# Kernel tuning notes

Measured on AMD Instinct MI355X. Metric: run time of the kernel, lower is better.

## Reference

```python
import jax, jax.numpy as jnp
import numpy as np

B, F, R, P, C = 2048, 64, 32, 16, 128  # batch, nfeature(dsym), nrole, npattern, dcontext
TAU = 2.0  # posn_attender sharpness


def setup_inputs() -> dict:
    key = jax.random.key(0)
    ks = jax.random.split(key, 16)
    w = lambda k, shape, s=0.05: jax.random.normal(k, shape, jnp.float32) * s
    z = lambda shape: jnp.zeros(shape, jnp.float32)
    return {
        "form": jax.random.normal(ks[0], (B, F, R), jnp.float32),
        "context": jax.random.normal(ks[1], (B, C), jnp.float32),
        "mod_W": w(ks[2], (C, P * 6)), "mod_b": z((P * 6,)),
        "wch_W": w(ks[3], (C, P * F)), "wch_b": z((P * F,)),
        "wdl_W": w(ks[4], (C, P)), "wdl_b": z((P,)),
        "wep_W": w(ks[5], (C, P * 4)), "wep_b": z((P * 4,)),
        "vch_W": w(ks[6], (C, P * F)), "vch_b": z((P * F,)),
        "vep_W": w(ks[7], (C, P * F * 4)), "vep_b": z((P * F * 4,)),
        "wnc_W": w(ks[8], (C, F)), "wnc_b": z((F,)),
        "wnd_W": w(ks[9], (C, 1)), "wnd_b": z((1,)),
        "wne_W": w(ks[10], (C, 1)), "wne_b": z((1,)),
        "m_W": w(ks[11], (3, C, P * F)), "m_Wb": z((3, P * F)),
        "mb_W": w(ks[12], (3, C, P)), "mb_b": z((3, P)),
    }


def _forward(form, context, mod_W, mod_b, wch_W, wch_b, wdl_W, wdl_b,
             wep_W, wep_b, vch_W, vch_b, vep_W, vep_b,
             wnc_W, wnc_b, wnd_W, wnd_b, wne_W, wne_b,
             m_W, m_Wb, mb_W, mb_b):
    nb = form.shape[0]
    lin = lambda W, b: context @ W + b

    # context-conditioned rule weights
    mod = jax.nn.softmax(lin(mod_W, mod_b).reshape(nb, P, 6), axis=-1)
    w_chng = mod[..., 0:1] * lin(wch_W, wch_b).reshape(nb, P, F)
    w_deln = mod[..., 1:2] * lin(wdl_W, wdl_b).reshape(nb, P, 1)
    w_epen = mod[..., 2:] * lin(wep_W, wep_b).reshape(nb, P, 4)
    v_chng = lin(vch_W, vch_b).reshape(nb, P, F)
    v_epen = lin(vep_W, vep_b).reshape(nb, P, F, 4)
    w_nochng = jnp.exp(lin(wnc_W, wnc_b))   # (B, F)
    w_nodeln = jnp.exp(lin(wnd_W, wnd_b))   # (B, 1)
    w_noepen = jnp.exp(lin(wne_W, wne_b))   # (B, 1)

    # Matcher3: trigram (prev, cur, next) feature matching; log-prob summed then exp'd
    prev = jnp.pad(form[:, :, :-1], ((0, 0), (0, 0), (1, 0)))
    nxt = jnp.pad(form[:, :, 1:], ((0, 0), (0, 0), (0, 1)))
    forms3 = jnp.stack([prev, form, nxt], 0)                                   # (3,B,F,R)
    Wk = (jnp.einsum('bc,kcn->kbn', context, m_W) + m_Wb[:, None, :]).reshape(3, nb, P, F)
    bk = jnp.einsum('bc,kcp->kbp', context, mb_W) + mb_b[:, None, :]
    score = jnp.einsum('kbpf,kbfr->kbpr', Wk, forms3) + bk[..., None]
    match = jnp.exp(jnp.sum(jax.nn.log_sigmoid(score), axis=0))                # (B,P,R)

    positions = jnp.arange(R, dtype=form.dtype)

    def posn_attn(posn):  # (B,1) soft position -> (B,R) radial-basis attention
        return jax.nn.softmax(-TAU * (posn - positions[None, :]) ** 2, axis=-1)

    def bind(out, x, attn):  # soft write symbol x at attended role
        a = attn[:, None, :]
        return out * (1.0 - a) + x[:, :, None] * a

    def epen(out, posn, match_i, we_p, ve_p):
        we = match_i * we_p                                                    # (B,P)
        p = jax.nn.sigmoid(jnp.sum(we, 1, keepdims=True) - w_noepen)           # (B,1)
        v = jnp.sum(jax.nn.relu(we)[..., None] * ve_p, 1)                      # (B,F)
        out_ = bind(out, v, posn_attn(posn))
        out = p[..., None] * out_ + (1.0 - p[..., None]) * out
        return out, posn + p

    def step(carry, x):
        out, posn = carry
        sym_i, match_i = x  # (B,F), (B,P)
        # epenthesis before
        out, posn = epen(out, posn, match_i, w_epen[..., 0], v_epen[..., 0])
        # feature change + deletion
        wc = match_i[..., None] * w_chng                                       # (B,P,F)
        p_chng = jax.nn.sigmoid(jnp.sum(wc, 1) - w_nochng)                     # (B,F)
        vc = jnp.sum(jax.nn.relu(wc) * v_chng, 1)                              # (B,F)
        sym = sym_i + p_chng * (vc - sym_i)
        out_ = bind(out, sym, posn_attn(posn))
        wd = match_i[..., None] * w_deln                                       # (B,P,1)
        p_deln = jax.nn.sigmoid(jnp.sum(wd, 1) - w_nodeln)                     # (B,1)
        out = (1.0 - p_deln[..., None]) * out_ + p_deln[..., None] * out
        posn = posn + (1.0 - p_deln)
        # epenthesis after
        out, posn = epen(out, posn, match_i, w_epen[..., 2], v_epen[..., 2])
        return (out, posn), None

    carry0 = (jnp.zeros((nb, F, R), form.dtype), jnp.zeros((nb, 1), form.dtype))
    xs = (jnp.moveaxis(form, 2, 0), jnp.moveaxis(match, 2, 0))
    (out, _), _ = jax.lax.scan(step, carry0, xs)
    return out


def reference(form, context, mod_W, mod_b, wch_W, wch_b, wdl_W, wdl_b,
              wep_W, wep_b, vch_W, vch_b, vep_W, vep_b,
              wnc_W, wnc_b, wnd_W, wnd_b, wne_W, wne_b,
              m_W, m_Wb, mb_W, mb_b):
    return _forward(form, context, mod_W, mod_b, wch_W, wch_b, wdl_W, wdl_b,
                    wep_W, wep_b, vch_W, vch_b, vep_W, vep_b,
                    wnc_W, wnc_b, wnd_W, wnd_b, wne_W, wne_b,
                    m_W, m_Wb, mb_W, mb_b)
```

## Files before the change

kernel.cpp:

```cpp
#include <hip/hip_runtime.h>

#define B_ 2048
#define NTOT 7426
#define YSTRIDE 7432
#define WSTRIDE 8192

typedef unsigned short u16;
typedef unsigned int   u32;
typedef __attribute__((ext_vector_type(2))) float v2f;

__device__ __forceinline__ float bfu(u16 u) {
    u32 i = ((u32)u) << 16; float f; __builtin_memcpy(&f, &i, 4); return f;
}
__device__ __forceinline__ float bflo(u32 w) {
    u32 i = w << 16; float f; __builtin_memcpy(&f, &i, 4); return f;
}
__device__ __forceinline__ float bfhi(u32 w) {
    u32 i = w & 0xffff0000u; float f; __builtin_memcpy(&f, &i, 4); return f;
}
__device__ __forceinline__ u16 f2bf(float v) {
    u32 iv; __builtin_memcpy(&iv, &v, 4);
    u32 r = (iv + 0x7fffu + ((iv >> 16) & 1u)) >> 16;
    return (u16)r;
}
__device__ __forceinline__ float sigm(float x) { return 1.f / (1.f + __expf(-x)); }
__device__ __forceinline__ float lsg(float x) {
    return fminf(x, 0.f) - log1pf(__expf(-fabsf(x)));
}

template<bool F32> __device__ __forceinline__ float LD(const void* p, int e) {
    if (F32) return ((const float*)p)[e];
    return bfu(((const u16*)p)[e]);
}
template<bool F32> __device__ __forceinline__ float2 LD2(const void* p, int e) {
    if (F32) { const float* q = (const float*)p; return make_float2(q[e], q[e + 1]); }
    u32 w = ((const u32*)p)[e >> 1];
    return make_float2(bflo(w), bfhi(w));
}
template<bool F32> __device__ __forceinline__ float4 LD4(const void* p, int e) {
    if (F32) return ((const float4*)p)[e >> 2];
    uint2 w = ((const uint2*)p)[e >> 2];
    return make_float4(bflo(w.x), bfhi(w.x), bflo(w.y), bfhi(w.y));
}
template<bool F32> __device__ __forceinline__ void ST(void* p, int e, float v) {
    if (F32) ((float*)p)[e] = v; else ((u16*)p)[e] = f2bf(v);
}

struct Args {
    const void *form, *ctx;
    const void *mod_W, *mod_b, *wch_W, *wch_b, *wdl_W, *wdl_b, *wep_W, *wep_b;
    const void *vch_W, *vch_b, *vep_W, *vep_b;
    const void *wnc_W, *wnc_b, *wnd_W, *wnd_b, *wne_W, *wne_b;
    const void *m_W, *m_Wb, *mb_W, *mb_b;
    void* outp;
};

__device__ __forceinline__ int probe_is_f32(const void* ctx, int t, int* flag_s) {
    if (t == 0) {
        int sane = 0;
        const u16* q = (const u16*)ctx;
        for (int i = 0; i < 64; ++i) {
            u16 u = q[2 * i];
            int ex = (u >> 7) & 0xFF;
            sane += (u == 0 || (ex >= 112 && ex <= 143)) ? 1 : 0;
        }
        *flag_s = (sane < 32) ? 1 : 0;
    }
    __syncthreads();
    return *flag_s;
}

struct PD { const void* p0; int off; int st; int mode; float b0, b1; };

template<bool F32>
__device__ __forceinline__ void resolve(const Args& A, int n0, PD& d) {
    if (n0 < 96) {
        d.mode = 0; d.p0 = A.mod_W; d.off = n0; d.st = 96;
        float2 b = LD2<F32>(A.mod_b, n0); d.b0 = b.x; d.b1 = b.y;
    } else if (n0 < 1120) {
        int j = n0 - 96;
        d.mode = 0; d.p0 = A.wch_W; d.off = j; d.st = 1024;
        float2 b = LD2<F32>(A.wch_b, j); d.b0 = b.x; d.b1 = b.y;
    } else if (n0 < 2144) {
        int j = n0 - 1120;
        d.mode = 0; d.p0 = A.vch_W; d.off = j; d.st = 1024;
        float2 b = LD2<F32>(A.vch_b, j); d.b0 = b.x; d.b1 = b.y;
    } else if (n0 < 4192) {
        int u = (n0 - 2144) >> 1;
        d.mode = 1; d.p0 = A.vep_W; d.off = 4 * u; d.st = 4096;
        float4 b = LD4<F32>(A.vep_b, 4 * u); d.b0 = b.x; d.b1 = b.z;
    } else if (n0 < 7264) {
        int i = n0 - 4192; int k = i >> 10, j = i & 1023;
        d.mode = 0; d.p0 = A.m_W; d.off = k * 131072 + j; d.st = 1024;
        float2 b = LD2<F32>(A.m_Wb, k * 1024 + j); d.b0 = b.x; d.b1 = b.y;
    } else if (n0 < 7312) {
        int i = n0 - 7264; int k = i >> 4, p = i & 15;
        d.mode = 0; d.p0 = A.mb_W; d.off = k * 2048 + p; d.st = 16;
        float2 b = LD2<F32>(A.mb_b, k * 16 + p); d.b0 = b.x; d.b1 = b.y;
    } else if (n0 < 7344) {
        int u = (n0 - 7312) >> 1;
        d.mode = 1; d.p0 = A.wep_W; d.off = 4 * u; d.st = 64;
        float4 b = LD4<F32>(A.wep_b, 4 * u); d.b0 = b.x; d.b1 = b.z;
    } else if (n0 < 7360) {
        int j = n0 - 7344;
        d.mode = 0; d.p0 = A.wdl_W; d.off = j; d.st = 16;
        float2 b = LD2<F32>(A.wdl_b, j); d.b0 = b.x; d.b1 = b.y;
    } else if (n0 < 7424) {
        int j = n0 - 7360;
        d.mode = 0; d.p0 = A.wnc_W; d.off = j; d.st = 64;
        float2 b = LD2<F32>(A.wnc_b, j); d.b0 = b.x; d.b1 = b.y;
    } else if (n0 == 7424) {
        d.mode = 2; d.p0 = A.wnd_W; d.off = 0; d.st = 1;
        d.b0 = LD<F32>(A.wnd_b, 0); d.b1 = LD<F32>(A.wne_b, 0);
    } else {
        d.mode = 3; d.p0 = A.mod_W; d.off = 0; d.st = 0; d.b0 = 0.f; d.b1 = 0.f;
    }
}

template<bool F32>
__device__ __forceinline__ v2f fetchw(const PD& d, const Args& A, int c) {
    if (d.mode == 0) {
        float2 w = LD2<F32>(d.p0, d.off + c * d.st);
        v2f r; r.x = w.x; r.y = w.y; return r;
    } else if (d.mode == 1) {
        float4 q = LD4<F32>(d.p0, d.off + c * d.st);
        v2f r; r.x = q.x; r.y = q.z; return r;
    } else if (d.mode == 2) {
        v2f r; r.x = LD<F32>(A.wnd_W, c); r.y = LD<F32>(A.wne_W, c); return r;
    }
    v2f r; r.x = 0.f; r.y = 0.f; return r;
}

template<bool F32>
__device__ void repack_body(int pid, const Args& A, float* Wcat, float* bcat) {
    int n0 = 2 * (pid & 4095);
    int c  = pid >> 12;
    PD d;
    resolve<F32>(A, n0, d);
    v2f w = fetchw<F32>(d, A, c);
    float2 s; s.x = w.x; s.y = w.y;
    *(float2*)(Wcat + (size_t)c * WSTRIDE + n0) = s;
    if (c == 0) { bcat[n0] = d.b0; bcat[n0 + 1] = d.b1; }
}

__global__ __launch_bounds__(256) void repack_kernel(Args A, float* Wcat, float* bcat) {
    __shared__ int dt_s;
    const int t = threadIdx.x;
    int isf32 = probe_is_f32(A.ctx, t, &dt_s);
    int pid = blockIdx.x * 256 + t;
    if (isf32) repack_body<true>(pid, A, Wcat, bcat);
    else       repack_body<false>(pid, A, Wcat, bcat);
}

template<bool F32>
__device__ void gemm4_body(float* ctx_s, int t, int blk, const void* __restrict__ ctx,
                           const float* __restrict__ Wcat, const float* __restrict__ bcat,
                           float* __restrict__ Y) {
    const int cb = blk & 7;
    const int mb = (blk >> 3) * 8;

    {
        int m = t >> 5, c0 = (t & 31) * 4;
        float4 v = LD4<F32>(ctx, (mb + m) * 128 + c0);
        *(float4*)&ctx_s[m * 128 + c0] = v;
    }
    __syncthreads();

    const int n0 = cb * 1024 + 4 * t;
    const float4* W4 = (const float4*)Wcat;
    const int wcol = n0 >> 2;

    float4 bv = *(const float4*)(bcat + n0);
    v2f acc[8][2];
    #pragma unroll
    for (int m = 0; m < 8; ++m) {
        acc[m][0].x = bv.x; acc[m][0].y = bv.y;
        acc[m][1].x = bv.z; acc[m][1].y = bv.w;
    }

    float4 w[4];
    #pragma unroll
    for (int j = 0; j < 4; ++j) w[j] = W4[(size_t)j * 2048 + wcol];

    #pragma unroll 1
    for (int c4 = 0; c4 < 128; c4 += 4) {
        float4 wn[4];
        if (c4 + 4 < 128) {
            #pragma unroll
            for (int j = 0; j < 4; ++j) wn[j] = W4[(size_t)(c4 + 4 + j) * 2048 + wcol];
        }
        #pragma unroll
        for (int m = 0; m < 8; ++m) {
            float4 cv = *(const float4*)&ctx_s[m * 128 + c4];
            float cs[4] = {cv.x, cv.y, cv.z, cv.w};
            #pragma unroll
            for (int j = 0; j < 4; ++j) {
                v2f cc; cc.x = cs[j]; cc.y = cs[j];
                v2f w01; w01.x = w[j].x; w01.y = w[j].y;
                v2f w23; w23.x = w[j].z; w23.y = w[j].w;
                acc[m][0] += cc * w01;
                acc[m][1] += cc * w23;
            }
        }
        #pragma unroll
        for (int j = 0; j < 4; ++j) w[j] = wn[j];
    }

    if (n0 < YSTRIDE) {
        #pragma unroll
        for (int m = 0; m < 8; ++m) {
            float4 s;
            s.x = acc[m][0].x; s.y = acc[m][0].y; s.z = acc[m][1].x; s.w = acc[m][1].y;
            *(float4*)(Y + (size_t)(mb + m) * YSTRIDE + n0) = s;
        }
    }
}

__global__ __launch_bounds__(256) void gemm4_kernel(Args A, const float* Wcat,
                                                    const float* bcat, float* Y) {
    __shared__ float ctx_s[8 * 128];
    __shared__ int dt_s;
    const int t = threadIdx.x, blk = blockIdx.x;
    int isf32 = probe_is_f32(A.ctx, t, &dt_s);
    if (isf32) gemm4_body<true>(ctx_s, t, blk, A.ctx, Wcat, bcat, Y);
    else       gemm4_body<false>(ctx_s, t, blk, A.ctx, Wcat, bcat, Y);
}

template<bool F32>
__device__ void gemm_body(float (*ctx_s)[128], int t, int blk, const Args& A, float* Y) {
    const int cb = blk & 3;
    const int mb = (blk >> 2) * 8;
    {
        int m = t >> 5, c0 = (t & 31) * 4;
        float4 v = LD4<F32>(A.ctx, (mb + m) * 128 + c0);
        ctx_s[m][c0] = v.x; ctx_s[m][c0 + 1] = v.y; ctx_s[m][c0 + 2] = v.z; ctx_s[m][c0 + 3] = v.w;
    }
    __syncthreads();
    PD d[4]; int n0[4];
    #pragma unroll
    for (int i = 0; i < 4; ++i) { n0[i] = cb * 2048 + i * 512 + 2 * t; resolve<F32>(A, n0[i], d[i]); }
    v2f acc[4][8];
    #pragma unroll
    for (int i = 0; i < 4; ++i)
        #pragma unroll
        for (int m = 0; m < 8; ++m) { acc[i][m].x = d[i].b0; acc[i][m].y = d[i].b1; }
    for (int c4 = 0; c4 < 32; ++c4) {
        float cv[8][4];
        #pragma unroll
        for (int m = 0; m < 8; ++m) *(float4*)cv[m] = *(const float4*)&ctx_s[m][c4 * 4];
        #pragma unroll
        for (int j = 0; j < 4; ++j) {
            int c = c4 * 4 + j;
            v2f w[4];
            #pragma unroll
            for (int i = 0; i < 4; ++i) w[i] = fetchw<F32>(d[i], A, c);
            #pragma unroll
            for (int m = 0; m < 8; ++m) {
                v2f cvv; cvv.x = cv[m][j]; cvv.y = cv[m][j];
                #pragma unroll
                for (int i = 0; i < 4; ++i) acc[i][m] += cvv * w[i];
            }
        }
    }
    #pragma unroll
    for (int i = 0; i < 4; ++i) {
        if (d[i].mode < 3) {
            #pragma unroll
            for (int m = 0; m < 8; ++m) {
                float2 s; s.x = acc[i][m].x; s.y = acc[i][m].y;
                *(float2*)(Y + (size_t)(mb + m) * YSTRIDE + n0[i]) = s;
            }
        }
    }
}

__global__ __launch_bounds__(256) void gemm_kernel(Args A, float* Y) {
    __shared__ float ctx_s[8][128];
    __shared__ int dt_s;
    const int t = threadIdx.x, blk = blockIdx.x;
    int isf32 = probe_is_f32(A.ctx, t, &dt_s);
    if (isf32) gemm_body<true>(ctx_s, t, blk, A, Y);
    else       gemm_body<false>(ctx_s, t, blk, A, Y);
}

struct __align__(16) ScanSmem {
    float U[6144];
    float V[3072];
    float match_s[512];
    float wnc_s[64];
    float wep0_s[16], wep2_s[16], wdl_s[16];
    float coef_s[96];
    float sc_s[2];
};

template<bool F32>
__device__ void scan_body(ScanSmem& S, int t, int b, const Args& A, const float* __restrict__ Y) {
    float* Wk_s   = S.U;
    float* bk_s   = S.U + 3072;
    float* modl   = S.U + 3120;
    float* form_s = S.U + 3312;
    float* xtab   = S.U;
    float* wch_s  = S.V;
    float* vch_s  = S.V + 1024;
    float* rlI    = S.V + 2048;
    float* gtab   = S.V;

    const float* Yr = Y + (size_t)b * YSTRIDE;
    const float4* Y4 = (const float4*)Yr;

    const int f_own = t & 63;
    const int fq    = t >> 6;

    const float2* vep2p = (const float2*)(Yr + 2144);
    v2f vepf[16];
    #pragma unroll
    for (int p = 0; p < 16; ++p) {
        float2 v = vep2p[p * 64 + f_own];
        vepf[p].x = v.x; vepf[p].y = v.y;
    }

    {
        int e0 = b * 2048 + t * 8;
        float4 x = LD4<F32>(A.form, e0);
        float4 y = LD4<F32>(A.form, e0 + 4);
        int f = t >> 2, r0 = (t & 3) * 8;
        float* dst = form_s + f * 33 + r0;
        dst[0] = x.x; dst[1] = x.y; dst[2] = x.z; dst[3] = x.w;
        dst[4] = y.x; dst[5] = y.y; dst[6] = y.z; dst[7] = y.w;
    }
    for (int i = t; i < 768; i += 256) ((float4*)Wk_s)[i] = Y4[1048 + i];
    if (t < 12) ((float4*)bk_s)[t] = Y4[1816 + t];
    if (t < 24) ((float4*)modl)[t] = Y4[t];
    ((float4*)wch_s)[t] = Y4[24 + t];
    ((float4*)vch_s)[t] = Y4[280 + t];
    if (t < 16) {
        S.wep0_s[t] = Yr[7312 + 2 * t];
        S.wep2_s[t] = Yr[7312 + 2 * t + 1];
        S.wdl_s[t]  = Yr[7344 + t];
    } else if (t >= 32 && t < 96) {
        S.wnc_s[t - 32] = __expf(Yr[7360 + (t - 32)]);
    } else if (t >= 96 && t < 98) {
        S.sc_s[t - 96] = __expf(Yr[7424 + (t - 96)]);
    }
    __syncthreads();

    if (t < 16) {
        float v[6]; float mx = -1e30f;
        #pragma unroll
        for (int j = 0; j < 6; ++j) { v[j] = modl[t * 6 + j]; mx = fmaxf(mx, v[j]); }
        float s = 0.f;
        #pragma unroll
        for (int j = 0; j < 6; ++j) { v[j] = __expf(v[j] - mx); s += v[j]; }
        float inv = 1.f / s;
        #pragma unroll
        for (int j = 0; j < 6; ++j) modl[t * 6 + j] = v[j] * inv;
    }
    __syncthreads();

    if (t < 16) {
        S.wep0_s[t] *= modl[t * 6 + 2];
        S.wep2_s[t] *= modl[t * 6 + 4];
        S.wdl_s[t]  *= modl[t * 6 + 1];
    }
    for (int i = t; i < 1024; i += 256) wch_s[i] *= modl[(i >> 6) * 6];

    const int my_r = t & 31;
    #pragma unroll 1
    for (int it = 0; it < 2; ++it) {
        int idx = t + 256 * it;
        int p = idx >> 5, r = idx & 31;
        float s0 = bk_s[p], s1 = bk_s[16 + p], s2 = bk_s[32 + p];
        const float4* w0 = (const float4*)(Wk_s + p * 64);
        const float4* w1 = (const float4*)(Wk_s + (16 + p) * 64);
        const float4* w2 = (const float4*)(Wk_s + (32 + p) * 64);
        for (int f4 = 0; f4 < 16; ++f4) {
            float a0[4], a1[4], a2[4];
            *(float4*)a0 = w0[f4]; *(float4*)a1 = w1[f4]; *(float4*)a2 = w2[f4];
            #pragma unroll
            for (int j = 0; j < 4; ++j) {
                int f = f4 * 4 + j;
                float f0 = form_s[f * 33 + r];
                float fm = __shfl_up(f0, 1, 32);   if (r == 0)  fm = 0.f;
                float fp = __shfl_down(f0, 1, 32); if (r == 31) fp = 0.f;
                s0 += a0[j] * fm; s1 += a1[j] * f0; s2 += a2[j] * fp;
            }
        }
        S.match_s[p * 32 + r] = __expf(lsg(s0) + lsg(s1) + lsg(s2));
    }
    __syncthreads();

    if (t < 96) {
        int sub = t >> 5, r = t & 31;
        const float* w = (sub == 0) ? S.wep0_s : (sub == 1) ? S.wdl_s : S.wep2_s;
        float s = 0.f;
        for (int p = 0; p < 16; ++p) s += S.match_s[p * 32 + r] * w[p];
        float cf;
        if (sub == 1) cf = 1.f - sigm(s - S.sc_s[0]);
        else          cf = sigm(s - S.sc_s[1]);
        S.coef_s[sub * 32 + r] = cf;
    }
    for (int i = t; i < 512; i += 256) {
        int p = i >> 5, r = i & 31;
        float m = S.match_s[p * 32 + r];
        rlI[2 * i]     = fmaxf(m * S.wep0_s[p], 0.f);
        rlI[2 * i + 1] = fmaxf(m * S.wep2_s[p], 0.f);
    }
    float wchf[16], vchf[16];
    #pragma unroll
    for (int p = 0; p < 16; ++p) {
        wchf[p] = wch_s[p * 64 + f_own];
        vchf[p] = vch_s[p * 64 + f_own];
    }
    const float wncf = S.wnc_s[f_own];
    float si_r[8];
    #pragma unroll
    for (int j = 0; j < 8; ++j) si_r[j] = form_s[f_own * 33 + fq * 8 + j];
    __syncthreads();

    #pragma unroll 1
    for (int j = 0; j < 8; ++j) {
        int rs = fq * 8 + j;
        v2f v02; v02.x = 0.f; v02.y = 0.f;
        float sum = 0.f, vs1 = 0.f;
        const v2f* rlp = (const v2f*)(rlI + 2 * rs);
        #pragma unroll
        for (int p = 0; p < 16; ++p) {
            v2f rl = rlp[p * 32];
            v02 += rl * vepf[p];
            float m = S.match_s[p * 32 + rs];
            float wc = m * wchf[p];
            sum += wc;
            vs1 += fmaxf(wc, 0.f) * vchf[p];
        }
        float pch = sigm(sum - wncf);
        float si  = si_r[j];
        xtab[0 * 2048 + rs * 64 + f_own] = v02.x;
        xtab[1 * 2048 + rs * 64 + f_own] = si + pch * (vs1 - si);
        xtab[2 * 2048 + rs * 64 + f_own] = v02.y;
    }
    __syncthreads();

    float* ck_s  = S.match_s;
    float* pos_s = S.match_s + 128;
    if (t < 96) ck_s[t] = S.coef_s[(t % 3) * 32 + (t / 3)];
    __syncthreads();
    if (t < 64) {
        float a = ck_s[t];
        float a0 = a;
        #pragma unroll
        for (int d = 1; d < 64; d <<= 1) { float v = __shfl_up(a, d, 64); if (t >= d) a += v; }
        pos_s[t] = a - a0;
        float carry = __shfl(a, 63, 64);
        float b2 = (t < 32) ? ck_s[64 + t] : 0.f;
        float c2 = b2;
        #pragma unroll
        for (int d = 1; d < 32; d <<= 1) { float v = __shfl_up(c2, d, 32); if ((t & 31) >= d) c2 += v; }
        if (t < 32) pos_s[64 + t] = carry + c2 - b2;
    }
    __syncthreads();

    #pragma unroll 1
    for (int i = 0; i < 12; ++i) {
        int idx = t + 256 * i;
        int k = idx >> 5, r = idx & 31;
        float posn = pos_s[k];
        float pc = fminf(posn, 31.f);
        float ci = floorf(pc + 0.5f);
        float dmin = posn - ci;
        float dd = posn - (float)r;
        float eo = __expf(-2.f * (dd * dd - dmin * dmin));
        float Z = eo;
        Z += __shfl_xor(Z, 1, 32);
        Z += __shfl_xor(Z, 2, 32);
        Z += __shfl_xor(Z, 4, 32);
        Z += __shfl_xor(Z, 8, 32);
        Z += __shfl_xor(Z, 16, 32);
        gtab[idx] = ck_s[k] * eo / Z;
    }
    __syncthreads();

    const int fgrp = t >> 5;
    v2f o01, o23, o45, o67;
    o01 = 0.f; o23 = 0.f; o45 = 0.f; o67 = 0.f;
    #pragma unroll 1
    for (int rs = 0; rs < 32; ++rs) {
        #pragma unroll
        for (int sub = 0; sub < 3; ++sub) {
            float g = gtab[(rs * 3 + sub) * 32 + my_r];
            v2f gv; gv.x = g; gv.y = g;
            const float4* xb = (const float4*)(xtab + sub * 2048 + rs * 64 + fgrp * 8);
            float4 xa = xb[0], xc = xb[1];
            v2f x01, x23, x45, x67;
            x01.x = xa.x; x01.y = xa.y; x23.x = xa.z; x23.y = xa.w;
            x45.x = xc.x; x45.y = xc.y; x67.x = xc.z; x67.y = xc.w;
            o01 += gv * (x01 - o01);
            o23 += gv * (x23 - o23);
            o45 += gv * (x45 - o45);
            o67 += gv * (x67 - o67);
        }
    }

    float oreg[8] = {o01.x, o01.y, o23.x, o23.y, o45.x, o45.y, o67.x, o67.y};
    #pragma unroll
    for (int i = 0; i < 8; ++i) {
        ST<F32>(A.outp, b * 2048 + (fgrp * 8 + i) * 32 + my_r, oreg[i]);
    }
}

__global__ __launch_bounds__(256) void scan_kernel(Args A, const float* Y) {
    __shared__ ScanSmem S;
    __shared__ int dt_s;
    const int t = threadIdx.x, b = blockIdx.x;
    int isf32 = probe_is_f32(A.ctx, t, &dt_s);
    if (isf32) scan_body<true>(S, t, b, A, Y);
    else       scan_body<false>(S, t, b, A, Y);
}

struct Smem {
    float U[6144];
    float form_s[64 * 33];
    float match_s[512];
    float wch_s[1024];
    float vch_s[1024];
    float vep0_s[1024];
    float vep2_s[1024];
    float wep0_s[16], wep2_s[16], wdl_s[16];
    float wnc_s[64];
    float sc_s[2];
    float ssum_s[96];
};

template<bool F32>
__device__ void mono_body(Smem& S, int t, int b, const Args& A) {
    float* c_s  = S.U;
    float* modl = S.U + 128;
    float* Wk_s = S.U + 224;
    float* bk_s = S.U + 3344;
    float* xtab = S.U;

    if (t < 128) c_s[t] = LD<F32>(A.ctx, b * 128 + t);
    {
        int e0 = b * 2048 + t * 8;
        float4 x = LD4<F32>(A.form, e0);
        float4 y = LD4<F32>(A.form, e0 + 4);
        int f = t >> 2, r0 = (t & 3) * 8;
        float* dst = S.form_s + f * 33 + r0;
        dst[0] = x.x; dst[1] = x.y; dst[2] = x.z; dst[3] = x.w;
        dst[4] = y.x; dst[5] = y.y; dst[6] = y.z; dst[7] = y.w;
    }
    __syncthreads();
    if (t < 96) {
        float a = LD<F32>(A.mod_b, t);
        for (int cc = 0; cc < 128; ++cc) a += c_s[cc] * LD<F32>(A.mod_W, cc * 96 + t);
        modl[t] = a;
    }
    __syncthreads();
    if (t < 16) {
        float v[6]; float mx = -1e30f;
        #pragma unroll
        for (int j = 0; j < 6; ++j) { v[j] = modl[t * 6 + j]; mx = fmaxf(mx, v[j]); }
        float s = 0.f;
        #pragma unroll
        for (int j = 0; j < 6; ++j) { v[j] = __expf(v[j] - mx); s += v[j]; }
        float inv = 1.f / s;
        #pragma unroll
        for (int j = 0; j < 6; ++j) modl[t * 6 + j] = v[j] * inv;
    }
    __syncthreads();
    for (int j = t; j < 512; j += 256) {
        int n0 = j * 2;
        float2 bb = LD2<F32>(A.wch_b, n0);
        float a0 = bb.x, a1 = bb.y;
        for (int cc = 0; cc < 128; ++cc) {
            float2 w = LD2<F32>(A.wch_W, cc * 1024 + n0); float cv = c_s[cc];
            a0 += cv * w.x; a1 += cv * w.y;
        }
        int p = n0 >> 6; float sc = modl[p * 6 + 0];
        S.wch_s[n0] = sc * a0; S.wch_s[n0 + 1] = sc * a1;
    }
    for (int j = t; j < 512; j += 256) {
        int n0 = j * 2;
        float2 bb = LD2<F32>(A.vch_b, n0);
        float a0 = bb.x, a1 = bb.y;
        for (int cc = 0; cc < 128; ++cc) {
            float2 w = LD2<F32>(A.vch_W, cc * 1024 + n0); float cv = c_s[cc];
            a0 += cv * w.x; a1 += cv * w.y;
        }
        S.vch_s[n0] = a0; S.vch_s[n0 + 1] = a1;
    }
    for (int u = t; u < 1024; u += 256) {
        int n0 = u * 4;
        float4 bb = LD4<F32>(A.vep_b, n0);
        float a0 = bb.x, a2 = bb.z;
        for (int cc = 0; cc < 128; ++cc) {
            float4 w = LD4<F32>(A.vep_W, cc * 4096 + n0); float cv = c_s[cc];
            a0 += cv * w.x; a2 += cv * w.z;
        }
        S.vep0_s[u] = a0; S.vep2_s[u] = a2;
    }
    for (int j = t; j < 1536; j += 256) {
        int k  = j >> 9;
        int jj = j & 511;
        int n0 = jj * 2;
        float2 bb = LD2<F32>(A.m_Wb, k * 1024 + n0);
        float a0 = bb.x, a1 = bb.y;
        for (int cc = 0; cc < 128; ++cc) {
            float2 w = LD2<F32>(A.m_W, (k * 128 + cc) * 1024 + n0); float cv = c_s[cc];
            a0 += cv * w.x; a1 += cv * w.y;
        }
        int p = n0 >> 6, f = n0 & 63;
        Wk_s[(k * 16 + p) * 65 + f]     = a0;
        Wk_s[(k * 16 + p) * 65 + f + 1] = a1;
    }
    if (t < 16) {
        int n0 = t * 4;
        float4 bb = LD4<F32>(A.wep_b, n0);
        float a0 = bb.x, a2 = bb.z;
        for (int cc = 0; cc < 128; ++cc) {
            float4 w = LD4<F32>(A.wep_W, cc * 64 + n0); float cv = c_s[cc];
            a0 += cv * w.x; a2 += cv * w.z;
        }
        S.wep0_s[t] = modl[t * 6 + 2] * a0;
        S.wep2_s[t] = modl[t * 6 + 4] * a2;
    } else if (t < 32) {
        int p = t - 16;
        float a = LD<F32>(A.wdl_b, p);
        for (int cc = 0; cc < 128; ++cc) a += c_s[cc] * LD<F32>(A.wdl_W, cc * 16 + p);
        S.wdl_s[p] = modl[p * 6 + 1] * a;
    } else if (t < 96) {
        int f = t - 32;
        float a = LD<F32>(A.wnc_b, f);
        for (int cc = 0; cc < 128; ++cc) a += c_s[cc] * LD<F32>(A.wnc_W, cc * 64 + f);
        S.wnc_s[f] = __expf(a);
    } else if (t < 98) {
        const void* W  = (t == 96) ? A.wnd_W : A.wne_W;
        const void* bb = (t == 96) ? A.wnd_b : A.wne_b;
        float a = LD<F32>(bb, 0);
        for (int cc = 0; cc < 128; ++cc) a += c_s[cc] * LD<F32>(W, cc);
        S.sc_s[t - 96] = __expf(a);
    } else if (t < 146) {
        int i = t - 98;
        int k = i >> 4, p = i & 15;
        float a = LD<F32>(A.mb_b, k * 16 + p);
        for (int cc = 0; cc < 128; ++cc) a += c_s[cc] * LD<F32>(A.mb_W, (k * 128 + cc) * 16 + p);
        bk_s[i] = a;
    }
    __syncthreads();
    for (int idx = t; idx < 512; idx += 256) {
        int p = idx >> 5, r = idx & 31;
        float s0 = bk_s[p], s1 = bk_s[16 + p], s2 = bk_s[32 + p];
        const float* w0 = Wk_s + p * 65;
        const float* w1 = Wk_s + (16 + p) * 65;
        const float* w2 = Wk_s + (32 + p) * 65;
        for (int f = 0; f < 64; ++f) {
            const float* fr = S.form_s + f * 33 + r;
            float fm1 = (r > 0)  ? fr[-1] : 0.f;
            float f0  = fr[0];
            float fp1 = (r < 31) ? fr[1]  : 0.f;
            s0 += w0[f] * fm1; s1 += w1[f] * f0; s2 += w2[f] * fp1;
        }
        S.match_s[p * 32 + r] = __expf(lsg(s0) + lsg(s1) + lsg(s2));
    }
    __syncthreads();
    if (t < 96) {
        int which = t >> 5, r = t & 31;
        const float* w = (which == 0) ? S.wep0_s : (which == 1) ? S.wep2_s : S.wdl_s;
        float s = 0.f;
        for (int p = 0; p < 16; ++p) s += S.match_s[p * 32 + r] * w[p];
        S.ssum_s[which * 32 + r] = s;
    }
    #pragma unroll 1
    for (int q = 0; q < 24; ++q) {
        int idx = t + 256 * q;
        int sub = idx >> 11;
        int rs  = (idx >> 6) & 31;
        int f   = idx & 63;
        float x;
        if (sub == 1) {
            float sum = 0.f, vs = 0.f;
            for (int p = 0; p < 16; ++p) {
                float wc = S.match_s[p * 32 + rs] * S.wch_s[p * 64 + f];
                sum += wc;
                vs  += fmaxf(wc, 0.f) * S.vch_s[p * 64 + f];
            }
            float pch = sigm(sum - S.wnc_s[f]);
            float si  = S.form_s[f * 33 + rs];
            x = si + pch * (vs - si);
        } else {
            const float* wep = (sub == 0) ? S.wep0_s : S.wep2_s;
            const float* vep = (sub == 0) ? S.vep0_s : S.vep2_s;
            float vs = 0.f;
            for (int p = 0; p < 16; ++p) {
                float w = S.match_s[p * 32 + rs] * wep[p];
                vs += fmaxf(w, 0.f) * vep[p * 64 + f];
            }
            x = vs;
        }
        xtab[idx] = x;
    }
    __syncthreads();
    const int my_r = t & 31;
    const int fgrp = t >> 5;
    float oreg[8];
    #pragma unroll
    for (int i = 0; i < 8; ++i) oreg[i] = 0.f;
    float posn = 0.f;
    const float wnd1v = S.sc_s[0];
    const float wne1v = S.sc_s[1];
    for (int rs = 0; rs < 32; ++rs) {
        #pragma unroll
        for (int sub = 0; sub < 3; ++sub) {
            float coef;
            if (sub == 1) coef = 1.f - sigm(S.ssum_s[64 + rs] - wnd1v);
            else          coef = sigm(S.ssum_s[(sub & 2) * 16 + rs] - wne1v);
            float pc = fminf(posn, 31.f);
            int ci = (int)(pc + 0.5f);
            int lo = ci - 4; if (lo < 0)  lo = 0;
            int hi = ci + 4; if (hi > 31) hi = 31;
            float dmin = posn - (float)ci;
            float mx = -2.f * dmin * dmin;
            float Z = 0.f, eo = 0.f;
            for (int r = lo; r <= hi; ++r) {
                float d = posn - (float)r;
                float e = __expf(-2.f * d * d - mx);
                Z += e;
                if (r == my_r) eo = e;
            }
            float g = coef * eo / Z;
            const float* xb = xtab + (sub * 2048 + rs * 64 + fgrp * 8);
            #pragma unroll
            for (int i = 0; i < 8; ++i) oreg[i] += g * (xb[i] - oreg[i]);
            posn += coef;
        }
    }
    #pragma unroll
    for (int i = 0; i < 8; ++i) {
        ST<F32>(A.outp, b * 2048 + (fgrp * 8 + i) * 32 + my_r, oreg[i]);
    }
}

__global__ __launch_bounds__(256) void phon_mono(Args A) {
    __shared__ Smem S;
    __shared__ int dt_s;
    const int t = threadIdx.x, b = blockIdx.x;
    int isf32 = probe_is_f32(A.ctx, t, &dt_s);
    if (isf32) mono_body<true>(S, t, b, A);
    else       mono_body<false>(S, t, b, A);
}

extern "C" void kernel_launch(void* const* d_in, const int* in_sizes, int n_in,
                              void* d_out, int out_size, void* d_ws, size_t ws_size,
                              hipStream_t stream) {
    Args A;
    A.form  = d_in[0];  A.ctx   = d_in[1];
    A.mod_W = d_in[2];  A.mod_b = d_in[3];
    A.wch_W = d_in[4];  A.wch_b = d_in[5];
    A.wdl_W = d_in[6];  A.wdl_b = d_in[7];
    A.wep_W = d_in[8];  A.wep_b = d_in[9];
    A.vch_W = d_in[10]; A.vch_b = d_in[11];
    A.vep_W = d_in[12]; A.vep_b = d_in[13];
    A.wnc_W = d_in[14]; A.wnc_b = d_in[15];
    A.wnd_W = d_in[16]; A.wnd_b = d_in[17];
    A.wne_W = d_in[18]; A.wne_b = d_in[19];
    A.m_W   = d_in[20]; A.m_Wb  = d_in[21];
    A.mb_W  = d_in[22]; A.mb_b  = d_in[23];
    A.outp  = d_out;

    const size_t needY = (size_t)B_ * YSTRIDE * sizeof(float);
    const size_t needW = needY + ((size_t)128 * WSTRIDE + WSTRIDE) * sizeof(float);
    if (ws_size >= needW) {
        float* Y    = (float*)d_ws;
        float* Wcat = Y + (size_t)B_ * YSTRIDE;
        float* bcat = Wcat + (size_t)128 * WSTRIDE;
        repack_kernel<<<(128 * WSTRIDE / 2) / 256, 256, 0, stream>>>(A, Wcat, bcat);
        gemm4_kernel<<<2048, 256, 0, stream>>>(A, Wcat, bcat, Y);
        scan_kernel<<<B_, 256, 0, stream>>>(A, Y);
    } else if (ws_size >= needY) {
        float* Y = (float*)d_ws;
        gemm_kernel<<<1024, 256, 0, stream>>>(A, Y);
        scan_kernel<<<B_, 256, 0, stream>>>(A, Y);
    } else {
        phon_mono<<<B_, 256, 0, stream>>>(A);
    }
}
```

Before: 274.1 us.

## Drop weight repack kernel, read weights directly, compute small projections in scan

Removes the repack kernel that built a concatenated weight matrix and instead has the GEMM kernel read each weight tensor directly, picking the source by column block (7 column groups of 1024). The small projections (mod, mb, wnc, wep, wdl, wnd, wne) are no longer part of the big GEMM; each scan block computes them per batch row from context in shared memory. This narrows the intermediate Y buffer and saves a kernel launch plus a full weight copy, at the cost of strided scalar weight loads inside the scan kernel and a strided vep read pattern in the GEMM.

```diff
diff --git a/kernel.cpp b/kernel.cpp
--- a/kernel.cpp
+++ b/kernel.cpp
@@ -1,9 +1,7 @@
 #include <hip/hip_runtime.h>
 
 #define B_ 2048
-#define NTOT 7426
-#define YSTRIDE 7432
-#define WSTRIDE 8192
+#define YS2 7168
 
 typedef unsigned short u16;
 typedef unsigned int   u32;
@@ -11,12 +9,6 @@
 
 __device__ __forceinline__ float bfu(u16 u) {
     u32 i = ((u32)u) << 16; float f; __builtin_memcpy(&f, &i, 4); return f;
-}
-__device__ __forceinline__ float bflo(u32 w) {
-    u32 i = w << 16; float f; __builtin_memcpy(&f, &i, 4); return f;
-}
-__device__ __forceinline__ float bfhi(u32 w) {
-    u32 i = w & 0xffff0000u; float f; __builtin_memcpy(&f, &i, 4); return f;
 }
 __device__ __forceinline__ u16 f2bf(float v) {
     u32 iv; __builtin_memcpy(&iv, &v, 4);
@@ -35,12 +27,18 @@
 template<bool F32> __device__ __forceinline__ float2 LD2(const void* p, int e) {
     if (F32) { const float* q = (const float*)p; return make_float2(q[e], q[e + 1]); }
     u32 w = ((const u32*)p)[e >> 1];
-    return make_float2(bflo(w), bfhi(w));
+    u32 lo = w << 16, hi = w & 0xffff0000u; float a, b;
+    __builtin_memcpy(&a, &lo, 4); __builtin_memcpy(&b, &hi, 4);
+    return make_float2(a, b);
 }
 template<bool F32> __device__ __forceinline__ float4 LD4(const void* p, int e) {
     if (F32) return ((const float4*)p)[e >> 2];
     uint2 w = ((const uint2*)p)[e >> 2];
-    return make_float4(bflo(w.x), bfhi(w.x), bflo(w.y), bfhi(w.y));
+    u32 a0 = w.x << 16, a1 = w.x & 0xffff0000u, a2 = w.y << 16, a3 = w.y & 0xffff0000u;
+    float f0, f1, f2, f3;
+    __builtin_memcpy(&f0, &a0, 4); __builtin_memcpy(&f1, &a1, 4);
+    __builtin_memcpy(&f2, &a2, 4); __builtin_memcpy(&f3, &a3, 4);
+    return make_float4(f0, f1, f2, f3);
 }
 template<bool F32> __device__ __forceinline__ void ST(void* p, int e, float v) {
     if (F32) ((float*)p)[e] = v; else ((u16*)p)[e] = f2bf(v);
@@ -70,107 +68,18 @@
     return *flag_s;
 }
 
-struct PD { const void* p0; int off; int st; int mode; float b0, b1; };
-
-template<bool F32>
-__device__ __forceinline__ void resolve(const Args& A, int n0, PD& d) {
-    if (n0 < 96) {
-        d.mode = 0; d.p0 = A.mod_W; d.off = n0; d.st = 96;
-        float2 b = LD2<F32>(A.mod_b, n0); d.b0 = b.x; d.b1 = b.y;
-    } else if (n0 < 1120) {
-        int j = n0 - 96;
-        d.mode = 0; d.p0 = A.wch_W; d.off = j; d.st = 1024;
-        float2 b = LD2<F32>(A.wch_b, j); d.b0 = b.x; d.b1 = b.y;
-    } else if (n0 < 2144) {
-        int j = n0 - 1120;
-        d.mode = 0; d.p0 = A.vch_W; d.off = j; d.st = 1024;
-        float2 b = LD2<F32>(A.vch_b, j); d.b0 = b.x; d.b1 = b.y;
-    } else if (n0 < 4192) {
-        int u = (n0 - 2144) >> 1;
-        d.mode = 1; d.p0 = A.vep_W; d.off = 4 * u; d.st = 4096;
-        float4 b = LD4<F32>(A.vep_b, 4 * u); d.b0 = b.x; d.b1 = b.z;
-    } else if (n0 < 7264) {
-        int i = n0 - 4192; int k = i >> 10, j = i & 1023;
-        d.mode = 0; d.p0 = A.m_W; d.off = k * 131072 + j; d.st = 1024;
-        float2 b = LD2<F32>(A.m_Wb, k * 1024 + j); d.b0 = b.x; d.b1 = b.y;
-    } else if (n0 < 7312) {
-        int i = n0 - 7264; int k = i >> 4, p = i & 15;
-        d.mode = 0; d.p0 = A.mb_W; d.off = k * 2048 + p; d.st = 16;
-        float2 b = LD2<F32>(A.mb_b, k * 16 + p); d.b0 = b.x; d.b1 = b.y;
-    } else if (n0 < 7344) {
-        int u = (n0 - 7312) >> 1;
-        d.mode = 1; d.p0 = A.wep_W; d.off = 4 * u; d.st = 64;
-        float4 b = LD4<F32>(A.wep_b, 4 * u); d.b0 = b.x; d.b1 = b.z;
-    } else if (n0 < 7360) {
-        int j = n0 - 7344;
-        d.mode = 0; d.p0 = A.wdl_W; d.off = j; d.st = 16;
-        float2 b = LD2<F32>(A.wdl_b, j); d.b0 = b.x; d.b1 = b.y;
-    } else if (n0 < 7424) {
-        int j = n0 - 7360;
-        d.mode = 0; d.p0 = A.wnc_W; d.off = j; d.st = 64;
-        float2 b = LD2<F32>(A.wnc_b, j); d.b0 = b.x; d.b1 = b.y;
-    } else if (n0 == 7424) {
-        d.mode = 2; d.p0 = A.wnd_W; d.off = 0; d.st = 1;
-        d.b0 = LD<F32>(A.wnd_b, 0); d.b1 = LD<F32>(A.wne_b, 0);
-    } else {
-        d.mode = 3; d.p0 = A.mod_W; d.off = 0; d.st = 0; d.b0 = 0.f; d.b1 = 0.f;
-    }
-}
-
-template<bool F32>
-__device__ __forceinline__ v2f fetchw(const PD& d, const Args& A, int c) {
-    if (d.mode == 0) {
-        float2 w = LD2<F32>(d.p0, d.off + c * d.st);
-        v2f r; r.x = w.x; r.y = w.y; return r;
-    } else if (d.mode == 1) {
-        float4 q = LD4<F32>(d.p0, d.off + c * d.st);
-        v2f r; r.x = q.x; r.y = q.z; return r;
-    } else if (d.mode == 2) {
-        v2f r; r.x = LD<F32>(A.wnd_W, c); r.y = LD<F32>(A.wne_W, c); return r;
-    }
-    v2f r; r.x = 0.f; r.y = 0.f; return r;
-}
-
-template<bool F32>
-__device__ void repack_body(int pid, const Args& A, float* Wcat, float* bcat) {
-    int n0 = 2 * (pid & 4095);
-    int c  = pid >> 12;
-    PD d;
-    resolve<F32>(A, n0, d);
-    v2f w = fetchw<F32>(d, A, c);
-    float2 s; s.x = w.x; s.y = w.y;
-    *(float2*)(Wcat + (size_t)c * WSTRIDE + n0) = s;
-    if (c == 0) { bcat[n0] = d.b0; bcat[n0 + 1] = d.b1; }
-}
-
-__global__ __launch_bounds__(256) void repack_kernel(Args A, float* Wcat, float* bcat) {
-    __shared__ int dt_s;
-    const int t = threadIdx.x;
-    int isf32 = probe_is_f32(A.ctx, t, &dt_s);
-    int pid = blockIdx.x * 256 + t;
-    if (isf32) repack_body<true>(pid, A, Wcat, bcat);
-    else       repack_body<false>(pid, A, Wcat, bcat);
-}
-
-template<bool F32>
-__device__ void gemm4_body(float* ctx_s, int t, int blk, const void* __restrict__ ctx,
-                           const float* __restrict__ Wcat, const float* __restrict__ bcat,
+template<bool F32, bool MB>
+__device__ __forceinline__ float4 ldw(const void* Wp, int soff, int c, int st) {
+    if (!MB) return LD4<F32>(Wp, soff + c * st);
+    float4 a = LD4<F32>(Wp, soff + c * 4096);
+    float4 b = LD4<F32>(Wp, soff + 4 + c * 4096);
+    return make_float4(a.x, a.z, b.x, b.z);
+}
+
+template<bool F32, bool MB>
+__device__ void gemm5_loop(const float* ctx_s, int t, int mb, int outc,
+                           const void* Wp, int soff, int st, float4 bv,
                            float* __restrict__ Y) {
-    const int cb = blk & 7;
-    const int mb = (blk >> 3) * 8;
-
-    {
-        int m = t >> 5, c0 = (t & 31) * 4;
-        float4 v = LD4<F32>(ctx, (mb + m) * 128 + c0);
-        *(float4*)&ctx_s[m * 128 + c0] = v;
-    }
-    __syncthreads();
-
-    const int n0 = cb * 1024 + 4 * t;
-    const float4* W4 = (const float4*)Wcat;
-    const int wcol = n0 >> 2;
-
-    float4 bv = *(const float4*)(bcat + n0);
     v2f acc[8][2];
     #pragma unroll
     for (int m = 0; m < 8; ++m) {
@@ -180,14 +89,14 @@
 
     float4 w[4];
     #pragma unroll
-    for (int j = 0; j < 4; ++j) w[j] = W4[(size_t)j * 2048 + wcol];
+    for (int j = 0; j < 4; ++j) w[j] = ldw<F32, MB>(Wp, soff, j, st);
 
     #pragma unroll 1
     for (int c4 = 0; c4 < 128; c4 += 4) {
         float4 wn[4];
         if (c4 + 4 < 128) {
             #pragma unroll
-            for (int j = 0; j < 4; ++j) wn[j] = W4[(size_t)(c4 + 4 + j) * 2048 + wcol];
+            for (int j = 0; j < 4; ++j) wn[j] = ldw<F32, MB>(Wp, soff, c4 + 4 + j, st);
         }
         #pragma unroll
         for (int m = 0; m < 8; ++m) {
@@ -206,81 +115,54 @@
         for (int j = 0; j < 4; ++j) w[j] = wn[j];
     }
 
-    if (n0 < YSTRIDE) {
-        #pragma unroll
-        for (int m = 0; m < 8; ++m) {
-            float4 s;
-            s.x = acc[m][0].x; s.y = acc[m][0].y; s.z = acc[m][1].x; s.w = acc[m][1].y;
-            *(float4*)(Y + (size_t)(mb + m) * YSTRIDE + n0) = s;
-        }
-    }
-}
-
-__global__ __launch_bounds__(256) void gemm4_kernel(Args A, const float* Wcat,
-                                                    const float* bcat, float* Y) {
+    #pragma unroll
+    for (int m = 0; m < 8; ++m) {
+        float4 s;
+        s.x = acc[m][0].x; s.y = acc[m][0].y; s.z = acc[m][1].x; s.w = acc[m][1].y;
+        *(float4*)(Y + (size_t)(mb + m) * YS2 + outc) = s;
+    }
+}
+
+template<bool F32>
+__device__ void gemm5_body(float* ctx_s, int t, int blk, const Args& A, float* Y) {
+    const int cc = blk % 7;
+    const int mb = (blk / 7) * 8;
+
+    {
+        int m = t >> 5, c0 = (t & 31) * 4;
+        float4 v = LD4<F32>(A.ctx, (mb + m) * 128 + c0);
+        *(float4*)&ctx_s[m * 128 + c0] = v;
+    }
+    __syncthreads();
+
+    const int outc = cc * 1024 + 4 * t;
+
+    if (cc == 2 || cc == 3) {
+        int soff = (cc - 2) * 2048 + 8 * t;
+        float4 ba = LD4<F32>(A.vep_b, soff);
+        float4 bb = LD4<F32>(A.vep_b, soff + 4);
+        float4 bv = make_float4(ba.x, ba.z, bb.x, bb.z);
+        gemm5_loop<F32, true>(ctx_s, t, mb, outc, A.vep_W, soff, 4096, bv, Y);
+    } else if (cc == 0) {
+        gemm5_loop<F32, false>(ctx_s, t, mb, outc, A.wch_W, 4 * t, 1024,
+                               LD4<F32>(A.wch_b, 4 * t), Y);
+    } else if (cc == 1) {
+        gemm5_loop<F32, false>(ctx_s, t, mb, outc, A.vch_W, 4 * t, 1024,
+                               LD4<F32>(A.vch_b, 4 * t), Y);
+    } else {
+        int k = cc - 4;
+        gemm5_loop<F32, false>(ctx_s, t, mb, outc, A.m_W, k * 131072 + 4 * t, 1024,
+                               LD4<F32>(A.m_Wb, k * 1024 + 4 * t), Y);
+    }
+}
+
+__global__ __launch_bounds__(256) void gemm5_kernel(Args A, float* Y) {
     __shared__ float ctx_s[8 * 128];
     __shared__ int dt_s;
     const int t = threadIdx.x, blk = blockIdx.x;
     int isf32 = probe_is_f32(A.ctx, t, &dt_s);
-    if (isf32) gemm4_body<true>(ctx_s, t, blk, A.ctx, Wcat, bcat, Y);
-    else       gemm4_body<false>(ctx_s, t, blk, A.ctx, Wcat, bcat, Y);
-}
-
-template<bool F32>
-__device__ void gemm_body(float (*ctx_s)[128], int t, int blk, const Args& A, float* Y) {
-    const int cb = blk & 3;
-    const int mb = (blk >> 2) * 8;
-    {
-        int m = t >> 5, c0 = (t & 31) * 4;
-        float4 v = LD4<F32>(A.ctx, (mb + m) * 128 + c0);
-        ctx_s[m][c0] = v.x; ctx_s[m][c0 + 1] = v.y; ctx_s[m][c0 + 2] = v.z; ctx_s[m][c0 + 3] = v.w;
-    }
-    __syncthreads();
-    PD d[4]; int n0[4];
-    #pragma unroll
-    for (int i = 0; i < 4; ++i) { n0[i] = cb * 2048 + i * 512 + 2 * t; resolve<F32>(A, n0[i], d[i]); }
-    v2f acc[4][8];
-    #pragma unroll
-    for (int i = 0; i < 4; ++i)
-        #pragma unroll
-        for (int m = 0; m < 8; ++m) { acc[i][m].x = d[i].b0; acc[i][m].y = d[i].b1; }
-    for (int c4 = 0; c4 < 32; ++c4) {
-        float cv[8][4];
-        #pragma unroll
-        for (int m = 0; m < 8; ++m) *(float4*)cv[m] = *(const float4*)&ctx_s[m][c4 * 4];
-        #pragma unroll
-        for (int j = 0; j < 4; ++j) {
-            int c = c4 * 4 + j;
-            v2f w[4];
-            #pragma unroll
-            for (int i = 0; i < 4; ++i) w[i] = fetchw<F32>(d[i], A, c);
-            #pragma unroll
-            for (int m = 0; m < 8; ++m) {
-                v2f cvv; cvv.x = cv[m][j]; cvv.y = cv[m][j];
-                #pragma unroll
-                for (int i = 0; i < 4; ++i) acc[i][m] += cvv * w[i];
-            }
-        }
-    }
-    #pragma unroll
-    for (int i = 0; i < 4; ++i) {
-        if (d[i].mode < 3) {
-            #pragma unroll
-            for (int m = 0; m < 8; ++m) {
-                float2 s; s.x = acc[i][m].x; s.y = acc[i][m].y;
-                *(float2*)(Y + (size_t)(mb + m) * YSTRIDE + n0[i]) = s;
-            }
-        }
-    }
-}
-
-__global__ __launch_bounds__(256) void gemm_kernel(Args A, float* Y) {
-    __shared__ float ctx_s[8][128];
-    __shared__ int dt_s;
-    const int t = threadIdx.x, blk = blockIdx.x;
-    int isf32 = probe_is_f32(A.ctx, t, &dt_s);
-    if (isf32) gemm_body<true>(ctx_s, t, blk, A, Y);
-    else       gemm_body<false>(ctx_s, t, blk, A, Y);
+    if (isf32) gemm5_body<true>(ctx_s, t, blk, A, Y);
+    else       gemm5_body<false>(ctx_s, t, blk, A, Y);
 }
 
 struct __align__(16) ScanSmem {
@@ -299,19 +181,20 @@
     float* bk_s   = S.U + 3072;
     float* modl   = S.U + 3120;
     float* form_s = S.U + 3312;
+    float* ctx_s  = S.U + 5424;
     float* xtab   = S.U;
     float* wch_s  = S.V;
     float* vch_s  = S.V + 1024;
     float* rlI    = S.V + 2048;
     float* gtab   = S.V;
 
-    const float* Yr = Y + (size_t)b * YSTRIDE;
+    const float* Yr = Y + (size_t)b * YS2;
     const float4* Y4 = (const float4*)Yr;
 
     const int f_own = t & 63;
     const int fq    = t >> 6;
 
-    const float2* vep2p = (const float2*)(Yr + 2144);
+    const float2* vep2p = (const float2*)(Yr + 2048);
     v2f vepf[16];
     #pragma unroll
     for (int p = 0; p < 16; ++p) {
@@ -328,19 +211,49 @@
         dst[0] = x.x; dst[1] = x.y; dst[2] = x.z; dst[3] = x.w;
         dst[4] = y.x; dst[5] = y.y; dst[6] = y.z; dst[7] = y.w;
     }
-    for (int i = t; i < 768; i += 256) ((float4*)Wk_s)[i] = Y4[1048 + i];
-    if (t < 12) ((float4*)bk_s)[t] = Y4[1816 + t];
-    if (t < 24) ((float4*)modl)[t] = Y4[t];
-    ((float4*)wch_s)[t] = Y4[24 + t];
-    ((float4*)vch_s)[t] = Y4[280 + t];
-    if (t < 16) {
-        S.wep0_s[t] = Yr[7312 + 2 * t];
-        S.wep2_s[t] = Yr[7312 + 2 * t + 1];
-        S.wdl_s[t]  = Yr[7344 + t];
-    } else if (t >= 32 && t < 96) {
-        S.wnc_s[t - 32] = __expf(Yr[7360 + (t - 32)]);
-    } else if (t >= 96 && t < 98) {
-        S.sc_s[t - 96] = __expf(Yr[7424 + (t - 96)]);
+    if (t < 32) {
+        float4 v = LD4<F32>(A.ctx, b * 128 + 4 * t);
+        *(float4*)&ctx_s[4 * t] = v;
+    }
+    for (int i = t; i < 768; i += 256) ((float4*)Wk_s)[i] = Y4[1024 + i];
+    ((float4*)wch_s)[t] = Y4[t];
+    ((float4*)vch_s)[t] = Y4[256 + t];
+    __syncthreads();
+
+    if (t < 96) {
+        float a = LD<F32>(A.mod_b, t);
+        for (int c = 0; c < 128; ++c) a += ctx_s[c] * LD<F32>(A.mod_W, c * 96 + t);
+        modl[t] = a;
+    } else if (t < 144) {
+        int i = t - 96; int k = i >> 4, p = i & 15;
+        float a = LD<F32>(A.mb_b, k * 16 + p);
+        for (int c = 0; c < 128; ++c) a += ctx_s[c] * LD<F32>(A.mb_W, (k * 128 + c) * 16 + p);
+        bk_s[i] = a;
+    } else if (t < 208) {
+        int f = t - 144;
+        float a = LD<F32>(A.wnc_b, f);
+        for (int c = 0; c < 128; ++c) a += ctx_s[c] * LD<F32>(A.wnc_W, c * 64 + f);
+        S.wnc_s[f] = __expf(a);
+    } else if (t < 224) {
+        int p = t - 208;
+        float a0 = LD<F32>(A.wep_b, 4 * p), a2 = LD<F32>(A.wep_b, 4 * p + 2);
+        for (int c = 0; c < 128; ++c) {
+            float cv = ctx_s[c];
+            a0 += cv * LD<F32>(A.wep_W, c * 64 + 4 * p);
+            a2 += cv * LD<F32>(A.wep_W, c * 64 + 4 * p + 2);
+        }
+        S.wep0_s[p] = a0; S.wep2_s[p] = a2;
+    } else if (t < 240) {
+        int p = t - 224;
+        float a = LD<F32>(A.wdl_b, p);
+        for (int c = 0; c < 128; ++c) a += ctx_s[c] * LD<F32>(A.wdl_W, c * 16 + p);
+        S.wdl_s[p] = a;
+    } else if (t < 242) {
+        const void* W  = (t == 240) ? A.wnd_W : A.wne_W;
+        const void* bb = (t == 240) ? A.wnd_b : A.wne_b;
+        float a = LD<F32>(bb, 0);
+        for (int c = 0; c < 128; ++c) a += ctx_s[c] * LD<F32>(W, c);
+        S.sc_s[t - 240] = __expf(a);
     }
     __syncthreads();
 
@@ -766,18 +679,10 @@
     A.mb_W  = d_in[22]; A.mb_b  = d_in[23];
     A.outp  = d_out;
 
-    const size_t needY = (size_t)B_ * YSTRIDE * sizeof(float);
-    const size_t needW = needY + ((size_t)128 * WSTRIDE + WSTRIDE) * sizeof(float);
-    if (ws_size >= needW) {
-        float* Y    = (float*)d_ws;
-        float* Wcat = Y + (size_t)B_ * YSTRIDE;
-        float* bcat = Wcat + (size_t)128 * WSTRIDE;
-        repack_kernel<<<(128 * WSTRIDE / 2) / 256, 256, 0, stream>>>(A, Wcat, bcat);
-        gemm4_kernel<<<2048, 256, 0, stream>>>(A, Wcat, bcat, Y);
-        scan_kernel<<<B_, 256, 0, stream>>>(A, Y);
-    } else if (ws_size >= needY) {
+    const size_t need = (size_t)B_ * YS2 * sizeof(float);
+    if (ws_size >= need) {
         float* Y = (float*)d_ws;
-        gemm_kernel<<<1024, 256, 0, stream>>>(A, Y);
+        gemm5_kernel<<<7 * 256, 256, 0, stream>>>(A, Y);
         scan_kernel<<<B_, 256, 0, stream>>>(A, Y);
     } else {
         phon_mono<<<B_, 256, 0, stream>>>(A);
```

After: 471.3 us. 71.9% more time.
